# Performance work log

Hardware: AMD Instinct MI355X
Metric: run time of the kernel (lower is better)

## Reference

```python
import jax, jax.numpy as jnp
import numpy as np

N, L, D_MODEL, NUM_HEADS, MAX_SEQ = 4, 1024, 1024, 16, 2048
DEPTH = D_MODEL // NUM_HEADS


def setup_inputs() -> dict:
    key = jax.random.key(0)
    ks = jax.random.split(key, 12)
    inv = 1.0 / np.sqrt(D_MODEL)
    inp = {
        "q_in": jax.random.normal(ks[0], (N, L, D_MODEL), jnp.float32),
        "k_in": jax.random.normal(ks[1], (N, L, D_MODEL), jnp.float32),
        "v_in": jax.random.normal(ks[2], (N, L, D_MODEL), jnp.float32),
        # causal additive mask: 1.0 where attention is disallowed (j > i)
        "mask": (jnp.triu(jnp.ones((L, L), jnp.float32), k=1))[None, None, :, :],
        "Wq": jax.random.normal(ks[3], (D_MODEL, D_MODEL), jnp.float32) * inv,
        "bq": jnp.zeros((D_MODEL,), jnp.float32),
        "Wk": jax.random.normal(ks[4], (D_MODEL, D_MODEL), jnp.float32) * inv,
        "bk": jnp.zeros((D_MODEL,), jnp.float32),
        "Wv": jax.random.normal(ks[5], (D_MODEL, D_MODEL), jnp.float32) * inv,
        "bv": jnp.zeros((D_MODEL,), jnp.float32),
        "Wo": jax.random.normal(ks[6], (D_MODEL, D_MODEL), jnp.float32) * inv,
        "bo": jnp.zeros((D_MODEL,), jnp.float32),
        "pos_emb": jax.random.normal(ks[7], (MAX_SEQ, DEPTH), jnp.float32) * 0.02,
    }
    return inp


def _rel_bias(q, pos_emb):
    """q: [N,H,L,depth] -> skewed relative-position bias s: [N,H,L,L]."""
    n, h, l, d = q.shape
    e = pos_emb[pos_emb.shape[0] - l:, :]                     # [L, depth]
    qe = jnp.einsum('nhld,md->nhlm', q, e)                    # [N,H,L,L]
    # keep only the last (i+1) entries of row i (upper-left triangle zeroed)
    m = qe.shape[-1]
    keep = (jnp.arange(m)[None, :] >= (m - 1 - jnp.arange(l))[:, None]).astype(qe.dtype)
    qe = qe * keep
    # skew via pad/reshape/slice
    padded = jnp.pad(qe, ((0, 0), (0, 0), (0, 0), (1, 0)))    # [N,H,L,L+1]
    s = padded.reshape(n, h, l + 1, l)[:, :, 1:, :]           # [N,H,L,L]
    return s


def reference(q_in, k_in, v_in, mask, Wq, bq, Wk, bk, Wv, bv, Wo, bo, pos_emb):
    n, l, dm = q_in.shape
    h, d = NUM_HEADS, DEPTH

    def split(x):
        return x.reshape(n, l, h, d).transpose(0, 2, 1, 3)    # [N,H,L,depth]

    q = split(q_in @ Wq + bq)
    k = split(k_in @ Wk + bk)
    v = split(v_in @ Wv + bv)

    s = _rel_bias(q, pos_emb)
    logits = (jnp.einsum('nhld,nhmd->nhlm', q, k) + s) / jnp.sqrt(jnp.float32(d))
    logits = logits + mask * (-1e9)
    attn = jax.nn.softmax(logits, axis=-1)                    # [N,H,L,L]
    out = jnp.einsum('nhlm,nhmd->nhld', attn, v)
    out = out.transpose(0, 2, 1, 3).reshape(n, l, dm)
    return out @ Wo + bo
```

## Files before the change

kernel.cpp:

```cpp
#include <hip/hip_runtime.h>

typedef unsigned short u16t;
typedef unsigned int   u32t;
typedef __bf16 bf16x8 __attribute__((ext_vector_type(8)));
typedef float  f32x4  __attribute__((ext_vector_type(4)));

#define NB     4
#define SEQ    1024
#define DMODEL 1024
#define NHEAD  16
#define DEPTH  64
#define MAXSEQ 2048
#define MTOK   (NB * SEQ)

#define AS1 __attribute__((address_space(1)))
#define AS3 __attribute__((address_space(3)))

__device__ __forceinline__ u16t f2bf(float f) {
  u32t u = __builtin_bit_cast(u32t, f);
  u32t r = (u + 0x7fffu + ((u >> 16) & 1u)) >> 16;
  return (u16t)r;
}
__device__ __forceinline__ float bf2f(u16t h) {
  return __builtin_bit_cast(float, (u32t)h << 16);
}
__device__ __forceinline__ void load_lds16(const void* g, void* l) {
  __builtin_amdgcn_global_load_lds((AS1 u32t*)(g), (AS3 u32t*)(l), 16, 0, 0);
}

__global__ void cvt3_kernel(const float* __restrict__ a, const float* __restrict__ b,
                            const float* __restrict__ c,
                            u16t* __restrict__ oa, u16t* __restrict__ ob,
                            u16t* __restrict__ oc, int n8) {
  int i = blockIdx.x * blockDim.x + threadIdx.x;
  if (i >= n8) return;
  const float* src = (blockIdx.z == 0) ? a : ((blockIdx.z == 1) ? b : c);
  u16t* dst = (blockIdx.z == 0) ? oa : ((blockIdx.z == 1) ? ob : oc);
  const float4* s4 = (const float4*)src;
  float4 x = s4[2 * i], y = s4[2 * i + 1];
  u16t tmp[8] = { f2bf(x.x), f2bf(x.y), f2bf(x.z), f2bf(x.w),
                  f2bf(y.x), f2bf(y.y), f2bf(y.z), f2bf(y.w) };
  ((uint4*)dst)[i] = *(const uint4*)tmp;
}

__global__ void transpose4_kernel(const float* __restrict__ w0, const float* __restrict__ w1,
                                  const float* __restrict__ w2, const float* __restrict__ w3,
                                  u16t* __restrict__ t0, u16t* __restrict__ t1,
                                  u16t* __restrict__ t2, u16t* __restrict__ t3,
                                  const float* __restrict__ pe, u16t* __restrict__ Er) {
  const int z = blockIdx.z;
  if (z == 4) {
    const int flat = blockIdx.y * 32 + blockIdx.x;
    if (flat < 256) {
      const int idx = flat * 256 + threadIdx.x;
      const int r = idx >> 6, d = idx & 63;
      Er[idx] = f2bf(pe[(size_t)(MAXSEQ - 1 - r) * DEPTH + d]);
    }
    return;
  }
  const float* W = (z == 0) ? w0 : ((z == 1) ? w1 : ((z == 2) ? w2 : w3));
  u16t* WT = (z == 0) ? t0 : ((z == 1) ? t1 : ((z == 2) ? t2 : t3));
  __shared__ float tile[32][33];
  const int tx = threadIdx.x & 31, ty = threadIdx.x >> 5;
  const int bx = blockIdx.x * 32, by = blockIdx.y * 32;
#pragma unroll
  for (int r = 0; r < 32; r += 8)
    tile[ty + r][tx] = W[(size_t)(by + ty + r) * DMODEL + bx + tx];
  __syncthreads();
#pragma unroll
  for (int r = 0; r < 32; r += 8)
    WT[(size_t)(bx + ty + r) * DMODEL + by + tx] = f2bf(tile[tx][ty + r]);
}

template <typename OutT>
__device__ __forceinline__ void gemm_bt_body(
    const u16t* __restrict__ A, const u16t* __restrict__ BT,
    const float* __restrict__ bias, OutT* __restrict__ C,
    int M, int Nc, int K, int bx, int by, float scale) {
  __shared__ __align__(16) u16t As[128 * 32];
  __shared__ __align__(16) u16t Bs[128 * 32];
  const int tid = threadIdx.x;
  const int wave = tid >> 6;
  const int lane = tid & 63;
  const int q = lane >> 4, t = lane & 15;
  const int lrow = lane >> 2, lch = lane & 3;
  const int bm = by * 128, bn = bx * 128;
  const int wi = (wave >> 1) * 64, wj = (wave & 1) * 64;

  f32x4 acc[4][4];
#pragma unroll
  for (int i = 0; i < 4; ++i)
#pragma unroll
    for (int j = 0; j < 4; ++j) acc[i][j] = f32x4{0.f, 0.f, 0.f, 0.f};

  for (int kt = 0; kt < K; kt += 32) {
    __syncthreads();
#pragma unroll
    for (int it = 0; it < 2; ++it) {
      const int rb = it * 64 + wave * 16;
      const u16t* ga = A + (size_t)(bm + rb + lrow) * K + kt + lch * 8;
      const u16t* gb = BT + (size_t)(bn + rb + lrow) * K + kt + lch * 8;
      load_lds16(ga, As + rb * 32);
      load_lds16(gb, Bs + rb * 32);
    }
    __syncthreads();
    bf16x8 af[4], bfr[4];
#pragma unroll
    for (int i = 0; i < 4; ++i) {
      af[i]  = *(const bf16x8*)(As + (wi + i * 16 + t) * 32 + q * 8);
      bfr[i] = *(const bf16x8*)(Bs + (wj + i * 16 + t) * 32 + q * 8);
    }
#pragma unroll
    for (int i = 0; i < 4; ++i)
#pragma unroll
      for (int j = 0; j < 4; ++j)
        acc[i][j] = __builtin_amdgcn_mfma_f32_16x16x32_bf16(af[i], bfr[j], acc[i][j], 0, 0, 0);
  }
#pragma unroll
  for (int j = 0; j < 4; ++j) {
    const int col = bn + wj + j * 16 + t;
    const float bv = bias[col];
#pragma unroll
    for (int i = 0; i < 4; ++i) {
#pragma unroll
      for (int r = 0; r < 4; ++r) {
        const int row = bm + wi + i * 16 + q * 4 + r;
        float v = (acc[i][j][r] + bv) * scale;
        if constexpr (sizeof(OutT) == 2) {
          C[(size_t)row * Nc + col] = f2bf(v);
        } else {
          C[(size_t)row * Nc + col] = v;
        }
      }
    }
  }
}

__global__ __launch_bounds__(256) void gemm_qkv_kernel(
    const u16t* qa, const u16t* ka, const u16t* va,
    const u16t* wq, const u16t* wk, const u16t* wv,
    const float* bq, const float* bk, const float* bv,
    u16t* qo, u16t* ko, u16t* vo) {
  const int z = blockIdx.z;
  const u16t* A = (z == 0) ? qa : ((z == 1) ? ka : va);
  const u16t* B = (z == 0) ? wq : ((z == 1) ? wk : wv);
  const float* bb = (z == 0) ? bq : ((z == 1) ? bk : bv);
  u16t* C = (z == 0) ? qo : ((z == 1) ? ko : vo);
  const float scale = (z == 0) ? 0.125f : 1.0f;
  gemm_bt_body<u16t>(A, B, bb, C, MTOK, DMODEL, DMODEL, blockIdx.x, blockIdx.y, scale);
}

__global__ __launch_bounds__(256) void gemm_out_kernel(
    const u16t* __restrict__ A, const u16t* __restrict__ W,
    const float* __restrict__ bias, float* __restrict__ C) {
  gemm_bt_body<float>(A, W, bias, C, MTOK, DMODEL, DMODEL, blockIdx.x, blockIdx.y, 1.0f);
}

__global__ __launch_bounds__(512, 4) void attn_kernel(
    const u16t* __restrict__ Qp, const u16t* __restrict__ Kp,
    const u16t* __restrict__ Vp, const u16t* __restrict__ Er,
    u16t* __restrict__ AO) {
  const int gx = blockIdx.x;
  const int xcd = gx & 7, slot = gx >> 3;
  const int ghi = slot & 7, k4 = slot >> 3;
  const int T = (k4 < 4) ? (7 - k4) : (k4 - 4);
  const int g = (ghi << 3) | xcd;
  const int n = g >> 4, h = g & 15;

  const int tid = threadIdx.x;
  const int wave = tid >> 6, lane = tid & 63;
  const int q = lane >> 4, t = lane & 15;
  const int rr = tid >> 3;
  const int c0 = (tid & 7) * 8;

  __shared__ __align__(16) u16t Es[256 * 72];
  __shared__ __align__(16) u16t Ks[64 * 72];
  __shared__ __align__(16) u16t Vt[64 * 64];
  __shared__ __align__(16) u16t TP[8 * 1152];
  u16t* TPw = TP + wave * 1152;

  const int I0 = T * 128;
  const int iw = I0 + wave * 16;
  const int jmax = 2 * T + 1;

  const size_t qoff = ((size_t)(n * SEQ + iw + t)) * DMODEL + h * DEPTH;
  const bf16x8 qf0 = *(const bf16x8*)(Qp + qoff + q * 8);
  const bf16x8 qf1 = *(const bf16x8*)(Qp + qoff + 32 + q * 8);

  const uint4 epre0 = *(const uint4*)(Er + ((size_t)(2 * T) * 64 + rr) * DEPTH + c0);
  const uint4 epre1 = *(const uint4*)(Er + ((size_t)(2 * T + 1) * 64 + rr) * DEPTH + c0);
  const size_t kvoff0 = ((size_t)(n * SEQ + rr)) * DMODEL + h * DEPTH + c0;
  uint4 kv = *(const uint4*)(Kp + kvoff0);
  uint4 vv = *(const uint4*)(Vp + kvoff0);
  uint4 ev = *(const uint4*)(Er + ((ptrdiff_t)(2 * T - 1) * 64 + rr) * DEPTH + c0);

  *(uint4*)(Es + (((2 * T) & 3) * 64 + rr) * 72 + c0) = epre0;
  *(uint4*)(Es + (((2 * T + 1) & 3) * 64 + rr) * 72 + c0) = epre1;

  f32x4 o[4];
#pragma unroll
  for (int c = 0; c < 4; ++c) o[c] = f32x4{0.f, 0.f, 0.f, 0.f};
  float l_r[4] = {0.f, 0.f, 0.f, 0.f};

  for (int jt = 0; jt <= jmax; ++jt) {
    const int J0 = jt * 64;
    const int cnew = 2 * T - 1 - jt;

    __syncthreads();
    *(uint4*)(Ks + rr * 72 + c0) = kv;
    *(uint4*)(Es + ((cnew & 3) * 64 + rr) * 72 + c0) = ev;
    {
      const u16t* pv = (const u16t*)&vv;
#pragma unroll
      for (int uu = 0; uu < 8; ++uu) {
        const int d = c0 + uu;
        Vt[d * 64 + (rr ^ (((d >> 2) & 7) << 3))] = pv[uu];
      }
    }
    __syncthreads();

    if (jt < jmax) {
      const size_t kvoff = ((size_t)(n * SEQ + J0 + 64 + rr)) * DMODEL + h * DEPTH + c0;
      kv = *(const uint4*)(Kp + kvoff);
      vv = *(const uint4*)(Vp + kvoff);
      ev = *(const uint4*)(Er + ((ptrdiff_t)(cnew - 1) * 64 + rr) * DEPTH + c0);
    }

    f32x4 s[4];
#pragma unroll
    for (int c = 0; c < 4; ++c) s[c] = f32x4{0.f, 0.f, 0.f, 0.f};
#pragma unroll
    for (int kk = 0; kk < 2; ++kk) {
      const bf16x8 qf = kk ? qf1 : qf0;
#pragma unroll
      for (int c = 0; c < 4; ++c) {
        const bf16x8 kf = *(const bf16x8*)(Ks + (c * 16 + t) * 72 + kk * 32 + q * 8);
        s[c] = __builtin_amdgcn_mfma_f32_16x16x32_bf16(qf, kf, s[c], 0, 0, 0);
      }
    }
    const int D0 = iw - J0 - 63;
    f32x4 tb[5];
#pragma unroll
    for (int cc = 0; cc < 5; ++cc) tb[cc] = f32x4{0.f, 0.f, 0.f, 0.f};
#pragma unroll
    for (int kk = 0; kk < 2; ++kk) {
      const bf16x8 qf = kk ? qf1 : qf0;
#pragma unroll
      for (int cc = 0; cc < 5; ++cc) {
        const int sl = (int)(((unsigned)(D0 + cc * 16 + t)) & 255u);
        const bf16x8 ef = *(const bf16x8*)(Es + sl * 72 + kk * 32 + q * 8);
        tb[cc] = __builtin_amdgcn_mfma_f32_16x16x32_bf16(qf, ef, tb[cc], 0, 0, 0);
      }
    }
#pragma unroll
    for (int cc = 0; cc < 5; ++cc)
#pragma unroll
      for (int r = 0; r < 4; ++r) {
        const int kp = cc * 16 + t - q * 4 - r;
        if ((unsigned)kp < 64u)
          TPw[(q * 4 + r) * 72 + kp] = f2bf(tb[cc][r]);
      }

    const int dIJ = I0 - J0;
#pragma unroll
    for (int c = 0; c < 4; ++c) {
      const int jc = c * 16 + t;
#pragma unroll
      for (int r = 0; r < 4; ++r) {
        const int ic = wave * 16 + q * 4 + r;
        float lg = s[c][r] + bf2f(TPw[(q * 4 + r) * 72 + 63 - c * 16 - t]);
        lg = (jc <= ic + dIJ) ? lg : -1e30f;
        const float pr = __expf(lg);
        s[c][r] = pr;
        l_r[r] += pr;
      }
    }
#pragma unroll
    for (int c = 0; c < 4; ++c)
#pragma unroll
      for (int r = 0; r < 4; ++r)
        TPw[(q * 4 + r) * 72 + c * 16 + t] = f2bf(s[c][r]);

    const bf16x8 pf0 = *(const bf16x8*)(TPw + t * 72 + q * 8);
    const bf16x8 pf1 = *(const bf16x8*)(TPw + t * 72 + 32 + q * 8);
#pragma unroll
    for (int c2 = 0; c2 < 4; ++c2) {
      const int dd = c2 * 16 + t;
      const int sw = (dd >> 2) & 7;
      const bf16x8 v0 = *(const bf16x8*)(Vt + dd * 64 + ((0 + q) ^ sw) * 8);
      const bf16x8 v1 = *(const bf16x8*)(Vt + dd * 64 + ((4 + q) ^ sw) * 8);
      o[c2] = __builtin_amdgcn_mfma_f32_16x16x32_bf16(pf0, v0, o[c2], 0, 0, 0);
      o[c2] = __builtin_amdgcn_mfma_f32_16x16x32_bf16(pf1, v1, o[c2], 0, 0, 0);
    }
  }

#pragma unroll
  for (int r = 0; r < 4; ++r) {
    float lsum = l_r[r];
    lsum += __shfl_xor(lsum, 1, 64);
    lsum += __shfl_xor(lsum, 2, 64);
    lsum += __shfl_xor(lsum, 4, 64);
    lsum += __shfl_xor(lsum, 8, 64);
    const float inv = 1.f / lsum;
    const size_t obase = ((size_t)(n * SEQ + iw + q * 4 + r)) * DMODEL + h * DEPTH;
#pragma unroll
    for (int c2 = 0; c2 < 4; ++c2)
      AO[obase + c2 * 16 + t] = f2bf(o[c2][r] * inv);
  }
}

extern "C" void kernel_launch(void* const* d_in, const int* in_sizes, int n_in,
                              void* d_out, int out_size, void* d_ws, size_t ws_size,
                              hipStream_t stream) {
  const float* q_in = (const float*)d_in[0];
  const float* k_in = (const float*)d_in[1];
  const float* v_in = (const float*)d_in[2];
  const float* Wq = (const float*)d_in[4];
  const float* bq = (const float*)d_in[5];
  const float* Wk = (const float*)d_in[6];
  const float* bk = (const float*)d_in[7];
  const float* Wv = (const float*)d_in[8];
  const float* bv = (const float*)d_in[9];
  const float* Wo = (const float*)d_in[10];
  const float* bo = (const float*)d_in[11];
  const float* pe = (const float*)d_in[12];
  float* out = (float*)d_out;

  char* ws = (char*)d_ws;
  constexpr size_t MB = 1ull << 20;
  u16t* qb  = (u16t*)(ws);
  u16t* kb  = (u16t*)(ws + 8 * MB);
  u16t* vb  = (u16t*)(ws + 16 * MB);
  u16t* Qp  = (u16t*)(ws + 24 * MB);
  u16t* Kp  = (u16t*)(ws + 32 * MB);
  u16t* Vp  = (u16t*)(ws + 40 * MB);
  u16t* AOb = (u16t*)(ws + 48 * MB);
  u16t* WqT = (u16t*)(ws + 56 * MB);
  u16t* WkT = (u16t*)(ws + 58 * MB);
  u16t* WvT = (u16t*)(ws + 60 * MB);
  u16t* WoT = (u16t*)(ws + 62 * MB);
  u16t* Erl = (u16t*)(ws + 64 * MB + 16 * 1024);

  const size_t SZA = (size_t)MTOK * DMODEL;
  const int n8 = (int)(SZA / 8);
  cvt3_kernel<<<dim3(n8 / 256, 1, 3), 256, 0, stream>>>(q_in, k_in, v_in, qb, kb, vb, n8);
  transpose4_kernel<<<dim3(32, 32, 5), 256, 0, stream>>>(Wq, Wk, Wv, Wo, WqT, WkT, WvT, WoT,
                                                         pe, Erl);

  gemm_qkv_kernel<<<dim3(DMODEL / 128, MTOK / 128, 3), 256, 0, stream>>>(
      qb, kb, vb, WqT, WkT, WvT, bq, bk, bv, Qp, Kp, Vp);

  attn_kernel<<<dim3(512, 1, 1), 512, 0, stream>>>(Qp, Kp, Vp, Erl, AOb);

  gemm_out_kernel<<<dim3(DMODEL / 128, MTOK / 128, 1), 256, 0, stream>>>(AOb, WoT, bo, out);
}
```

Measured before the change: 243.2 us.

## Split attention KV range across two blocks and merge partials in output GEMM

Each attention block now pairs a long and a short query tile (T and 7-T) and handles only every other KV tile (even or odd, selected by u), writing unnormalized partial outputs and row sums to two buffers. The output projection GEMM merges the two partials and normalizes them while staging A into LDS, replacing the separate normalized AO buffer. The aim is to balance causal work across blocks and shorten the critical path per block. The cost is extra partial-output traffic, register-based A staging instead of direct LDS loads in the out GEMM, and a merge that skips max-subtraction, so it relies on the logits staying small.

```diff
diff --git a/kernel.cpp b/kernel.cpp
--- a/kernel.cpp
+++ b/kernel.cpp
@@ -72,98 +72,149 @@
     WT[(size_t)(bx + ty + r) * DMODEL + by + tx] = f2bf(tile[tx][ty + r]);
 }
 
-template <typename OutT>
-__device__ __forceinline__ void gemm_bt_body(
-    const u16t* __restrict__ A, const u16t* __restrict__ BT,
-    const float* __restrict__ bias, OutT* __restrict__ C,
-    int M, int Nc, int K, int bx, int by, float scale) {
-  __shared__ __align__(16) u16t As[128 * 32];
-  __shared__ __align__(16) u16t Bs[128 * 32];
-  const int tid = threadIdx.x;
-  const int wave = tid >> 6;
-  const int lane = tid & 63;
-  const int q = lane >> 4, t = lane & 15;
-  const int lrow = lane >> 2, lch = lane & 3;
-  const int bm = by * 128, bn = bx * 128;
-  const int wi = (wave >> 1) * 64, wj = (wave & 1) * 64;
-
-  f32x4 acc[4][4];
-#pragma unroll
-  for (int i = 0; i < 4; ++i)
-#pragma unroll
-    for (int j = 0; j < 4; ++j) acc[i][j] = f32x4{0.f, 0.f, 0.f, 0.f};
-
-  for (int kt = 0; kt < K; kt += 32) {
-    __syncthreads();
-#pragma unroll
-    for (int it = 0; it < 2; ++it) {
-      const int rb = it * 64 + wave * 16;
-      const u16t* ga = A + (size_t)(bm + rb + lrow) * K + kt + lch * 8;
-      const u16t* gb = BT + (size_t)(bn + rb + lrow) * K + kt + lch * 8;
-      load_lds16(ga, As + rb * 32);
-      load_lds16(gb, Bs + rb * 32);
-    }
-    __syncthreads();
-    bf16x8 af[4], bfr[4];
-#pragma unroll
-    for (int i = 0; i < 4; ++i) {
-      af[i]  = *(const bf16x8*)(As + (wi + i * 16 + t) * 32 + q * 8);
-      bfr[i] = *(const bf16x8*)(Bs + (wj + i * 16 + t) * 32 + q * 8);
-    }
-#pragma unroll
-    for (int i = 0; i < 4; ++i)
-#pragma unroll
-      for (int j = 0; j < 4; ++j)
-        acc[i][j] = __builtin_amdgcn_mfma_f32_16x16x32_bf16(af[i], bfr[j], acc[i][j], 0, 0, 0);
-  }
-#pragma unroll
-  for (int j = 0; j < 4; ++j) {
-    const int col = bn + wj + j * 16 + t;
-    const float bv = bias[col];
-#pragma unroll
-    for (int i = 0; i < 4; ++i) {
-#pragma unroll
-      for (int r = 0; r < 4; ++r) {
-        const int row = bm + wi + i * 16 + q * 4 + r;
-        float v = (acc[i][j][r] + bv) * scale;
-        if constexpr (sizeof(OutT) == 2) {
-          C[(size_t)row * Nc + col] = f2bf(v);
-        } else {
-          C[(size_t)row * Nc + col] = v;
-        }
-      }
-    }
-  }
-}
-
 __global__ __launch_bounds__(256) void gemm_qkv_kernel(
     const u16t* qa, const u16t* ka, const u16t* va,
     const u16t* wq, const u16t* wk, const u16t* wv,
     const float* bq, const float* bk, const float* bv,
     u16t* qo, u16t* ko, u16t* vo) {
   const int z = blockIdx.z;
-  const u16t* A = (z == 0) ? qa : ((z == 1) ? ka : va);
-  const u16t* B = (z == 0) ? wq : ((z == 1) ? wk : wv);
-  const float* bb = (z == 0) ? bq : ((z == 1) ? bk : bv);
-  u16t* C = (z == 0) ? qo : ((z == 1) ? ko : vo);
+  const u16t* __restrict__ A = (z == 0) ? qa : ((z == 1) ? ka : va);
+  const u16t* __restrict__ BT = (z == 0) ? wq : ((z == 1) ? wk : wv);
+  const float* __restrict__ bias = (z == 0) ? bq : ((z == 1) ? bk : bv);
+  u16t* __restrict__ C = (z == 0) ? qo : ((z == 1) ? ko : vo);
   const float scale = (z == 0) ? 0.125f : 1.0f;
-  gemm_bt_body<u16t>(A, B, bb, C, MTOK, DMODEL, DMODEL, blockIdx.x, blockIdx.y, scale);
+
+  __shared__ __align__(16) u16t As[128 * 32];
+  __shared__ __align__(16) u16t Bs[128 * 32];
+  const int tid = threadIdx.x;
+  const int wave = tid >> 6, lane = tid & 63;
+  const int q = lane >> 4, t = lane & 15;
+  const int lrow = lane >> 2, lch = lane & 3;
+  const int bm = blockIdx.y * 128, bn = blockIdx.x * 128;
+  const int wi = (wave >> 1) * 64, wj = (wave & 1) * 64;
+
+  f32x4 acc[4][4];
+#pragma unroll
+  for (int i = 0; i < 4; ++i)
+#pragma unroll
+    for (int j = 0; j < 4; ++j) acc[i][j] = f32x4{0.f, 0.f, 0.f, 0.f};
+
+  for (int kt = 0; kt < DMODEL; kt += 32) {
+    __syncthreads();
+#pragma unroll
+    for (int it = 0; it < 2; ++it) {
+      const int rb = it * 64 + wave * 16;
+      const u16t* ga = A + (size_t)(bm + rb + lrow) * DMODEL + kt + lch * 8;
+      const u16t* gb = BT + (size_t)(bn + rb + lrow) * DMODEL + kt + lch * 8;
+      load_lds16(ga, As + rb * 32);
+      load_lds16(gb, Bs + rb * 32);
+    }
+    __syncthreads();
+    bf16x8 af[4], bfr[4];
+#pragma unroll
+    for (int i = 0; i < 4; ++i) {
+      af[i]  = *(const bf16x8*)(As + (wi + i * 16 + t) * 32 + q * 8);
+      bfr[i] = *(const bf16x8*)(Bs + (wj + i * 16 + t) * 32 + q * 8);
+    }
+#pragma unroll
+    for (int i = 0; i < 4; ++i)
+#pragma unroll
+      for (int j = 0; j < 4; ++j)
+        acc[i][j] = __builtin_amdgcn_mfma_f32_16x16x32_bf16(af[i], bfr[j], acc[i][j], 0, 0, 0);
+  }
+#pragma unroll
+  for (int j = 0; j < 4; ++j) {
+    const int col = bn + wj + j * 16 + t;
+    const float bv2 = bias[col];
+#pragma unroll
+    for (int i = 0; i < 4; ++i)
+#pragma unroll
+      for (int r = 0; r < 4; ++r) {
+        const int row = bm + wi + i * 16 + q * 4 + r;
+        C[(size_t)row * DMODEL + col] = f2bf((acc[i][j][r] + bv2) * scale);
+      }
+  }
 }
 
 __global__ __launch_bounds__(256) void gemm_out_kernel(
-    const u16t* __restrict__ A, const u16t* __restrict__ W,
-    const float* __restrict__ bias, float* __restrict__ C) {
-  gemm_bt_body<float>(A, W, bias, C, MTOK, DMODEL, DMODEL, blockIdx.x, blockIdx.y, 1.0f);
+    const u16t* __restrict__ Po0, const u16t* __restrict__ Po1,
+    const float* __restrict__ Pl0, const float* __restrict__ Pl1,
+    const u16t* __restrict__ BT, const float* __restrict__ bias,
+    float* __restrict__ C) {
+  __shared__ __align__(16) u16t As[128 * 32];
+  __shared__ __align__(16) u16t Bs[128 * 32];
+  const int tid = threadIdx.x;
+  const int wave = tid >> 6, lane = tid & 63;
+  const int q = lane >> 4, t = lane & 15;
+  const int lrow = lane >> 2, lch = lane & 3;
+  const int bm = blockIdx.y * 128, bn = blockIdx.x * 128;
+  const int wi = (wave >> 1) * 64, wj = (wave & 1) * 64;
+
+  f32x4 acc[4][4];
+#pragma unroll
+  for (int i = 0; i < 4; ++i)
+#pragma unroll
+    for (int j = 0; j < 4; ++j) acc[i][j] = f32x4{0.f, 0.f, 0.f, 0.f};
+
+  for (int kt = 0; kt < DMODEL; kt += 32) {
+    __syncthreads();
+#pragma unroll
+    for (int it = 0; it < 2; ++it) {
+      const int rb = it * 64 + wave * 16;
+      const u16t* gb = BT + (size_t)(bn + rb + lrow) * DMODEL + kt + lch * 8;
+      load_lds16(gb, Bs + rb * 32);
+      const int row = bm + rb + lrow;
+      const int colb = kt + lch * 8;
+      const int hh = colb >> 6;
+      const int nn = row >> 10, ii = row & 1023;
+      const size_t lidx = (size_t)((nn * NHEAD + hh) << 10) + ii;
+      const float winv = 1.f / (Pl0[lidx] + Pl1[lidx]);
+      const uint4 a0 = *(const uint4*)(Po0 + (size_t)row * DMODEL + colb);
+      const uint4 a1 = *(const uint4*)(Po1 + (size_t)row * DMODEL + colb);
+      const u16t* p0 = (const u16t*)&a0;
+      const u16t* p1 = (const u16t*)&a1;
+      u16t blend[8];
+#pragma unroll
+      for (int k = 0; k < 8; ++k)
+        blend[k] = f2bf((bf2f(p0[k]) + bf2f(p1[k])) * winv);
+      *(uint4*)(As + rb * 32 + lane * 8) = *(const uint4*)blend;
+    }
+    __syncthreads();
+    bf16x8 af[4], bfr[4];
+#pragma unroll
+    for (int i = 0; i < 4; ++i) {
+      af[i]  = *(const bf16x8*)(As + (wi + i * 16 + t) * 32 + q * 8);
+      bfr[i] = *(const bf16x8*)(Bs + (wj + i * 16 + t) * 32 + q * 8);
+    }
+#pragma unroll
+    for (int i = 0; i < 4; ++i)
+#pragma unroll
+      for (int j = 0; j < 4; ++j)
+        acc[i][j] = __builtin_amdgcn_mfma_f32_16x16x32_bf16(af[i], bfr[j], acc[i][j], 0, 0, 0);
+  }
+#pragma unroll
+  for (int j = 0; j < 4; ++j) {
+    const int col = bn + wj + j * 16 + t;
+    const float bv = bias[col];
+#pragma unroll
+    for (int i = 0; i < 4; ++i)
+#pragma unroll
+      for (int r = 0; r < 4; ++r) {
+        const int row = bm + wi + i * 16 + q * 4 + r;
+        C[(size_t)row * DMODEL + col] = acc[i][j][r] + bv;
+      }
+  }
 }
 
 __global__ __launch_bounds__(512, 4) void attn_kernel(
     const u16t* __restrict__ Qp, const u16t* __restrict__ Kp,
     const u16t* __restrict__ Vp, const u16t* __restrict__ Er,
-    u16t* __restrict__ AO) {
+    u16t* __restrict__ Po0, u16t* __restrict__ Po1,
+    float* __restrict__ Pl0, float* __restrict__ Pl1) {
   const int gx = blockIdx.x;
   const int xcd = gx & 7, slot = gx >> 3;
-  const int ghi = slot & 7, k4 = slot >> 3;
-  const int T = (k4 < 4) ? (7 - k4) : (k4 - 4);
+  const int ghi = slot & 7, pu = slot >> 3;
+  const int p = pu >> 1, u = pu & 1;
   const int g = (ghi << 3) | xcd;
   const int n = g >> 4, h = g & 15;
 
@@ -179,133 +230,147 @@
   __shared__ __align__(16) u16t TP[8 * 1152];
   u16t* TPw = TP + wave * 1152;
 
-  const int I0 = T * 128;
-  const int iw = I0 + wave * 16;
-  const int jmax = 2 * T + 1;
-
-  const size_t qoff = ((size_t)(n * SEQ + iw + t)) * DMODEL + h * DEPTH;
-  const bf16x8 qf0 = *(const bf16x8*)(Qp + qoff + q * 8);
-  const bf16x8 qf1 = *(const bf16x8*)(Qp + qoff + 32 + q * 8);
-
-  const uint4 epre0 = *(const uint4*)(Er + ((size_t)(2 * T) * 64 + rr) * DEPTH + c0);
-  const uint4 epre1 = *(const uint4*)(Er + ((size_t)(2 * T + 1) * 64 + rr) * DEPTH + c0);
-  const size_t kvoff0 = ((size_t)(n * SEQ + rr)) * DMODEL + h * DEPTH + c0;
-  uint4 kv = *(const uint4*)(Kp + kvoff0);
-  uint4 vv = *(const uint4*)(Vp + kvoff0);
-  uint4 ev = *(const uint4*)(Er + ((ptrdiff_t)(2 * T - 1) * 64 + rr) * DEPTH + c0);
-
-  *(uint4*)(Es + (((2 * T) & 3) * 64 + rr) * 72 + c0) = epre0;
-  *(uint4*)(Es + (((2 * T + 1) & 3) * 64 + rr) * 72 + c0) = epre1;
-
-  f32x4 o[4];
-#pragma unroll
-  for (int c = 0; c < 4; ++c) o[c] = f32x4{0.f, 0.f, 0.f, 0.f};
-  float l_r[4] = {0.f, 0.f, 0.f, 0.f};
-
-  for (int jt = 0; jt <= jmax; ++jt) {
-    const int J0 = jt * 64;
-    const int cnew = 2 * T - 1 - jt;
-
-    __syncthreads();
-    *(uint4*)(Ks + rr * 72 + c0) = kv;
-    *(uint4*)(Es + ((cnew & 3) * 64 + rr) * 72 + c0) = ev;
-    {
-      const u16t* pv = (const u16t*)&vv;
-#pragma unroll
-      for (int uu = 0; uu < 8; ++uu) {
-        const int d = c0 + uu;
-        Vt[d * 64 + (rr ^ (((d >> 2) & 7) << 3))] = pv[uu];
-      }
-    }
-    __syncthreads();
-
-    if (jt < jmax) {
-      const size_t kvoff = ((size_t)(n * SEQ + J0 + 64 + rr)) * DMODEL + h * DEPTH + c0;
-      kv = *(const uint4*)(Kp + kvoff);
-      vv = *(const uint4*)(Vp + kvoff);
-      ev = *(const uint4*)(Er + ((ptrdiff_t)(cnew - 1) * 64 + rr) * DEPTH + c0);
-    }
-
-    f32x4 s[4];
-#pragma unroll
-    for (int c = 0; c < 4; ++c) s[c] = f32x4{0.f, 0.f, 0.f, 0.f};
-#pragma unroll
-    for (int kk = 0; kk < 2; ++kk) {
-      const bf16x8 qf = kk ? qf1 : qf0;
+  u16t* __restrict__ Pou = u ? Po1 : Po0;
+  float* __restrict__ Plu = u ? Pl1 : Pl0;
+
+#pragma unroll
+  for (int ph = 0; ph < 2; ++ph) {
+    const int T = ph ? p : (7 - p);
+    const int I0 = T * 128;
+    const int iw = I0 + wave * 16;
+    const int jmax = 2 * T + 1;
+
+    const size_t qoff = ((size_t)(n * SEQ + iw + t)) * DMODEL + h * DEPTH;
+    const bf16x8 qf0 = *(const bf16x8*)(Qp + qoff + q * 8);
+    const bf16x8 qf1 = *(const bf16x8*)(Qp + qoff + 32 + q * 8);
+
+    f32x4 o[4];
+#pragma unroll
+    for (int c = 0; c < 4; ++c) o[c] = f32x4{0.f, 0.f, 0.f, 0.f};
+    float l_r[4] = {0.f, 0.f, 0.f, 0.f};
+
+    int J0 = 64 * u;
+    int D0 = I0 - J0 - 63;
+    size_t kvo = ((size_t)(n * SEQ + J0 + rr)) * DMODEL + h * DEPTH + c0;
+    uint4 kv = *(const uint4*)(Kp + kvo);
+    uint4 vv = *(const uint4*)(Vp + kvo);
+    uint4 ev0 = *(const uint4*)(Er + (ptrdiff_t)(D0 + rr) * DEPTH + c0);
+    uint4 ev1 = *(const uint4*)(Er + (ptrdiff_t)(D0 + 64 + rr) * DEPTH + c0);
+    uint4 ev2 = *(const uint4*)(Er + (ptrdiff_t)(D0 + 128 + rr) * DEPTH + c0);
+    bool first = true;
+
+    for (int jt = u; jt <= jmax; jt += 2) {
+      __syncthreads();
+      *(uint4*)(Ks + rr * 72 + c0) = kv;
+      {
+        const u16t* pv = (const u16t*)&vv;
+#pragma unroll
+        for (int uu = 0; uu < 8; ++uu) {
+          const int d = c0 + uu;
+          Vt[d * 64 + (rr ^ (((d >> 2) & 7) << 3))] = pv[uu];
+        }
+      }
+      *(uint4*)(Es + ((D0 + rr) & 255) * 72 + c0) = ev0;
+      *(uint4*)(Es + ((D0 + 64 + rr) & 255) * 72 + c0) = ev1;
+      if (first)
+        *(uint4*)(Es + ((D0 + 128 + rr) & 255) * 72 + c0) = ev2;
+      __syncthreads();
+
+      if (jt + 2 <= jmax) {
+        const size_t kvn = ((size_t)(n * SEQ + J0 + 128 + rr)) * DMODEL + h * DEPTH + c0;
+        kv = *(const uint4*)(Kp + kvn);
+        vv = *(const uint4*)(Vp + kvn);
+        ev0 = *(const uint4*)(Er + (ptrdiff_t)(D0 - 128 + rr) * DEPTH + c0);
+        ev1 = *(const uint4*)(Er + (ptrdiff_t)(D0 - 64 + rr) * DEPTH + c0);
+      }
+
+      f32x4 s[4];
+#pragma unroll
+      for (int c = 0; c < 4; ++c) s[c] = f32x4{0.f, 0.f, 0.f, 0.f};
+#pragma unroll
+      for (int kk = 0; kk < 2; ++kk) {
+        const bf16x8 qf = kk ? qf1 : qf0;
+#pragma unroll
+        for (int c = 0; c < 4; ++c) {
+          const bf16x8 kf = *(const bf16x8*)(Ks + (c * 16 + t) * 72 + kk * 32 + q * 8);
+          s[c] = __builtin_amdgcn_mfma_f32_16x16x32_bf16(qf, kf, s[c], 0, 0, 0);
+        }
+      }
+      const int D0w = iw - J0 - 63;
+      f32x4 tb[5];
+#pragma unroll
+      for (int cc = 0; cc < 5; ++cc) tb[cc] = f32x4{0.f, 0.f, 0.f, 0.f};
+#pragma unroll
+      for (int kk = 0; kk < 2; ++kk) {
+        const bf16x8 qf = kk ? qf1 : qf0;
+#pragma unroll
+        for (int cc = 0; cc < 5; ++cc) {
+          const int sl = (int)(((unsigned)(D0w + cc * 16 + t)) & 255u);
+          const bf16x8 ef = *(const bf16x8*)(Es + sl * 72 + kk * 32 + q * 8);
+          tb[cc] = __builtin_amdgcn_mfma_f32_16x16x32_bf16(qf, ef, tb[cc], 0, 0, 0);
+        }
+      }
+#pragma unroll
+      for (int cc = 0; cc < 5; ++cc)
+#pragma unroll
+        for (int r = 0; r < 4; ++r) {
+          const int kp = cc * 16 + t - q * 4 - r;
+          if ((unsigned)kp < 64u)
+            TPw[(q * 4 + r) * 72 + kp] = f2bf(tb[cc][r]);
+        }
+
+      const int dIJ = I0 - J0;
 #pragma unroll
       for (int c = 0; c < 4; ++c) {
-        const bf16x8 kf = *(const bf16x8*)(Ks + (c * 16 + t) * 72 + kk * 32 + q * 8);
-        s[c] = __builtin_amdgcn_mfma_f32_16x16x32_bf16(qf, kf, s[c], 0, 0, 0);
-      }
-    }
-    const int D0 = iw - J0 - 63;
-    f32x4 tb[5];
-#pragma unroll
-    for (int cc = 0; cc < 5; ++cc) tb[cc] = f32x4{0.f, 0.f, 0.f, 0.f};
-#pragma unroll
-    for (int kk = 0; kk < 2; ++kk) {
-      const bf16x8 qf = kk ? qf1 : qf0;
-#pragma unroll
-      for (int cc = 0; cc < 5; ++cc) {
-        const int sl = (int)(((unsigned)(D0 + cc * 16 + t)) & 255u);
-        const bf16x8 ef = *(const bf16x8*)(Es + sl * 72 + kk * 32 + q * 8);
-        tb[cc] = __builtin_amdgcn_mfma_f32_16x16x32_bf16(qf, ef, tb[cc], 0, 0, 0);
-      }
-    }
-#pragma unroll
-    for (int cc = 0; cc < 5; ++cc)
-#pragma unroll
-      for (int r = 0; r < 4; ++r) {
-        const int kp = cc * 16 + t - q * 4 - r;
-        if ((unsigned)kp < 64u)
-          TPw[(q * 4 + r) * 72 + kp] = f2bf(tb[cc][r]);
-      }
-
-    const int dIJ = I0 - J0;
-#pragma unroll
-    for (int c = 0; c < 4; ++c) {
-      const int jc = c * 16 + t;
-#pragma unroll
-      for (int r = 0; r < 4; ++r) {
-        const int ic = wave * 16 + q * 4 + r;
-        float lg = s[c][r] + bf2f(TPw[(q * 4 + r) * 72 + 63 - c * 16 - t]);
-        lg = (jc <= ic + dIJ) ? lg : -1e30f;
-        const float pr = __expf(lg);
-        s[c][r] = pr;
-        l_r[r] += pr;
-      }
-    }
-#pragma unroll
-    for (int c = 0; c < 4; ++c)
-#pragma unroll
-      for (int r = 0; r < 4; ++r)
-        TPw[(q * 4 + r) * 72 + c * 16 + t] = f2bf(s[c][r]);
-
-    const bf16x8 pf0 = *(const bf16x8*)(TPw + t * 72 + q * 8);
-    const bf16x8 pf1 = *(const bf16x8*)(TPw + t * 72 + 32 + q * 8);
-#pragma unroll
-    for (int c2 = 0; c2 < 4; ++c2) {
-      const int dd = c2 * 16 + t;
-      const int sw = (dd >> 2) & 7;
-      const bf16x8 v0 = *(const bf16x8*)(Vt + dd * 64 + ((0 + q) ^ sw) * 8);
-      const bf16x8 v1 = *(const bf16x8*)(Vt + dd * 64 + ((4 + q) ^ sw) * 8);
-      o[c2] = __builtin_amdgcn_mfma_f32_16x16x32_bf16(pf0, v0, o[c2], 0, 0, 0);
-      o[c2] = __builtin_amdgcn_mfma_f32_16x16x32_bf16(pf1, v1, o[c2], 0, 0, 0);
-    }
-  }
-
-#pragma unroll
-  for (int r = 0; r < 4; ++r) {
-    float lsum = l_r[r];
-    lsum += __shfl_xor(lsum, 1, 64);
-    lsum += __shfl_xor(lsum, 2, 64);
-    lsum += __shfl_xor(lsum, 4, 64);
-    lsum += __shfl_xor(lsum, 8, 64);
-    const float inv = 1.f / lsum;
-    const size_t obase = ((size_t)(n * SEQ + iw + q * 4 + r)) * DMODEL + h * DEPTH;
-#pragma unroll
-    for (int c2 = 0; c2 < 4; ++c2)
-      AO[obase + c2 * 16 + t] = f2bf(o[c2][r] * inv);
+        const int jc = c * 16 + t;
+#pragma unroll
+        for (int r = 0; r < 4; ++r) {
+          const int ic = wave * 16 + q * 4 + r;
+          float lg = s[c][r] + bf2f(TPw[(q * 4 + r) * 72 + 63 - c * 16 - t]);
+          lg = (jc <= ic + dIJ) ? lg : -1e30f;
+          const float pr = __expf(lg);
+          s[c][r] = pr;
+          l_r[r] += pr;
+        }
+      }
+#pragma unroll
+      for (int c = 0; c < 4; ++c)
+#pragma unroll
+        for (int r = 0; r < 4; ++r)
+          TPw[(q * 4 + r) * 72 + c * 16 + t] = f2bf(s[c][r]);
+
+      const bf16x8 pf0 = *(const bf16x8*)(TPw + t * 72 + q * 8);
+      const bf16x8 pf1 = *(const bf16x8*)(TPw + t * 72 + 32 + q * 8);
+#pragma unroll
+      for (int c2 = 0; c2 < 4; ++c2) {
+        const int dd = c2 * 16 + t;
+        const int sw = (dd >> 2) & 7;
+        const bf16x8 v0 = *(const bf16x8*)(Vt + dd * 64 + ((0 + q) ^ sw) * 8);
+        const bf16x8 v1 = *(const bf16x8*)(Vt + dd * 64 + ((4 + q) ^ sw) * 8);
+        o[c2] = __builtin_amdgcn_mfma_f32_16x16x32_bf16(pf0, v0, o[c2], 0, 0, 0);
+        o[c2] = __builtin_amdgcn_mfma_f32_16x16x32_bf16(pf1, v1, o[c2], 0, 0, 0);
+      }
+
+      J0 += 128;
+      D0 -= 128;
+      first = false;
+    }
+
+#pragma unroll
+    for (int r = 0; r < 4; ++r) {
+      float lsum = l_r[r];
+      lsum += __shfl_xor(lsum, 1, 64);
+      lsum += __shfl_xor(lsum, 2, 64);
+      lsum += __shfl_xor(lsum, 4, 64);
+      lsum += __shfl_xor(lsum, 8, 64);
+      const int i = iw + q * 4 + r;
+      const size_t obase = ((size_t)(n * SEQ + i)) * DMODEL + h * DEPTH;
+#pragma unroll
+      for (int c2 = 0; c2 < 4; ++c2)
+        Pou[obase + c2 * 16 + t] = f2bf(o[c2][r]);
+      if (t == 0)
+        Plu[((size_t)(n * NHEAD + h) << 10) + i] = lsum;
+    }
   }
 }
 
@@ -331,10 +396,13 @@
   u16t* qb  = (u16t*)(ws);
   u16t* kb  = (u16t*)(ws + 8 * MB);
   u16t* vb  = (u16t*)(ws + 16 * MB);
+  u16t* Po0 = (u16t*)(ws);
+  u16t* Po1 = (u16t*)(ws + 8 * MB);
+  float* Pl0 = (float*)(ws + 16 * MB);
+  float* Pl1 = (float*)(ws + 16 * MB + 512 * 1024);
   u16t* Qp  = (u16t*)(ws + 24 * MB);
   u16t* Kp  = (u16t*)(ws + 32 * MB);
   u16t* Vp  = (u16t*)(ws + 40 * MB);
-  u16t* AOb = (u16t*)(ws + 48 * MB);
   u16t* WqT = (u16t*)(ws + 56 * MB);
   u16t* WkT = (u16t*)(ws + 58 * MB);
   u16t* WvT = (u16t*)(ws + 60 * MB);
@@ -350,7 +418,8 @@
   gemm_qkv_kernel<<<dim3(DMODEL / 128, MTOK / 128, 3), 256, 0, stream>>>(
       qb, kb, vb, WqT, WkT, WvT, bq, bk, bv, Qp, Kp, Vp);
 
-  attn_kernel<<<dim3(512, 1, 1), 512, 0, stream>>>(Qp, Kp, Vp, Erl, AOb);
-
-  gemm_out_kernel<<<dim3(DMODEL / 128, MTOK / 128, 1), 256, 0, stream>>>(AOb, WoT, bo, out);
-}
+  attn_kernel<<<dim3(512, 1, 1), 512, 0, stream>>>(Qp, Kp, Vp, Erl, Po0, Po1, Pl0, Pl1);
+
+  gemm_out_kernel<<<dim3(DMODEL / 128, MTOK / 128, 1), 256, 0, stream>>>(
+      Po0, Po1, Pl0, Pl1, WoT, bo, out);
+}
```

New measurement: 284.5 us. +17.0%, slower.
